# Optimization experiments

Measured on AMD Instinct MI355X. Metric: run time of the kernel, lower is better.

## Reference

```python
import jax, jax.numpy as jnp
import numpy as np

EPS = 1e-8  # torch CosineSimilarity eps
TEMP = 0.05

def _l2norm(x):
    n = jnp.sqrt(jnp.sum(x * x, axis=-1, keepdims=True))
    return x / jnp.maximum(n, EPS)

def setup_inputs() -> dict:
    key = jax.random.key(0)
    k1, k2, k3 = jax.random.split(key, 3)
    query = jax.random.normal(k1, (256, 768), dtype=jnp.float32)
    keys = jax.random.normal(k2, (256, 768), dtype=jnp.float32)
    queue = jax.random.normal(k3, (64, 1024, 768), dtype=jnp.float32)
    return {"query": query, "keys": keys, "queue": queue}

def reference(query, keys, queue):
    B, D = query.shape
    qn = _l2norm(query)                       # [B, D]
    kn = _l2norm(keys)                        # [B, D]
    negn = _l2norm(queue.reshape(-1, D))      # [N, D]
    sim_pos = jnp.einsum('bd,cd->bc', qn, kn)   # [B, B]
    sim_neg = jnp.einsum('bd,nd->bn', qn, negn) # [B, N]
    logits = jnp.concatenate([sim_pos, sim_neg], axis=1) / TEMP  # [B, B+N]
    target = jnp.arange(B)
    logp = jax.nn.log_softmax(logits, axis=-1)
    loss = -jnp.mean(logp[jnp.arange(B), target])
    return loss
```

## Files before the change

kernel.cpp:

```cpp
#include <hip/hip_runtime.h>
#include <hip/hip_bf16.h>

typedef __attribute__((ext_vector_type(8))) short short8;
typedef __attribute__((ext_vector_type(4))) float f32x4;

#define TEMP_INV 20.0f
#define NCH 256

__device__ inline unsigned short f2bf(float f){
    unsigned int u = __builtin_bit_cast(unsigned int, f);
    u += 0x7fffu + ((u >> 16) & 1u);
    return (unsigned short)(u >> 16);
}
__device__ inline float bf2f(unsigned short h){
    unsigned int u = ((unsigned int)h) << 16;
    return __builtin_bit_cast(float, u);
}
__device__ inline unsigned int pk2bf(float a, float b){
    return (unsigned int)f2bf(a) | ((unsigned int)f2bf(b) << 16);
}

#define GLOAD16(src, dst) __builtin_amdgcn_global_load_lds( \
    (const __attribute__((address_space(1))) unsigned int*)(src), \
    (__attribute__((address_space(3))) unsigned int*)(dst), 16, 0, 0)

__global__ __launch_bounds__(256) void k_norm(const float* __restrict__ q,
                                              unsigned short* __restrict__ Aswz,
                                              float* __restrict__ out){
    int b = blockIdx.x, t = threadIdx.x;
    if (b == 0 && t == 0) out[0] = 0.f;
    const float* qr = q + b * 768;
    float v0 = qr[t], v1 = qr[t + 256], v2 = qr[t + 512];
    float ss = v0*v0 + v1*v1 + v2*v2;
#pragma unroll
    for (int o = 32; o; o >>= 1) ss += __shfl_xor(ss, o);
    __shared__ float red[4];
    if ((t & 63) == 0) red[t >> 6] = ss;
    __syncthreads();
    ss = red[0] + red[1] + red[2] + red[3];
    float inv = 1.0f / fmaxf(sqrtf(ss), 1e-8f);
    float nv[3] = {v0 * inv, v1 * inv, v2 * inv};
#pragma unroll
    for (int j = 0; j < 3; j++){
        int cc = t + 256 * j;
        unsigned short h = f2bf(nv[j]);
        int kc = cc >> 6, kl = cc & 63, g = kl >> 3, e = kl & 7;
        int slot = g ^ (b & 7);
        Aswz[kc * 16384 + b * 64 + slot * 8 + e] = h;
    }
}

__global__ __launch_bounds__(1024) void k_main(
        const float* __restrict__ keys,
        const float* __restrict__ queue,
        const unsigned short* __restrict__ Aswz,
        float* __restrict__ pmax,
        float* __restrict__ psum,
        float* __restrict__ diag){
    __shared__ unsigned short Atile[16384];
    __shared__ unsigned short Btile[16384];
    __shared__ unsigned short bxn16[768];
    __shared__ float invn[256];
    __shared__ float redm[4][256];
    __shared__ float reds[4][256];
    __shared__ float xred[4][256];
    __shared__ float wred[16];
    __shared__ float sxs;

    const int b = blockIdx.x, t = threadIdx.x;
    const int lane = t & 63;
    const int w = t >> 6;
    const int wm = w >> 2, wn = w & 3;
    const int frow = lane & 15, fg = lane >> 4;
    const int c = t >> 2, q4 = t & 3;
    const int c7 = c & 7;

    {
        float v = (t < 768) ? keys[b * 768 + t] : 0.f;
        float ssx = v * v;
#pragma unroll
        for (int o = 32; o; o >>= 1) ssx += __shfl_xor(ssx, o);
        if (lane == 0) wred[w] = ssx;
        __syncthreads();
        if (t == 0){
            float s = 0.f;
#pragma unroll
            for (int i = 0; i < 16; i++) s += wred[i];
            sxs = 1.0f / fmaxf(sqrtf(s), 1e-8f);
        }
        __syncthreads();
        if (t < 768) bxn16[t] = f2bf(v * sxs);
        __syncthreads();
    }

    const float* rp = queue + (size_t)(b * 256 + c) * 768 + q4 * 16;
    const int xrow = t & 255, xk = t >> 8;

    float ssq = 0.f, dx = 0.f;
    f32x4 acc[4][4];
#pragma unroll
    for (int i = 0; i < 4; i++)
#pragma unroll
        for (int j = 0; j < 4; j++) acc[i][j] = (f32x4)0.f;

    for (int kc = 0; kc < 12; ++kc){
        if (kc) __syncthreads();
        GLOAD16(Aswz + kc * 16384 + t * 8, Atile + t * 8);
        GLOAD16(Aswz + kc * 16384 + 8192 + t * 8, Atile + 8192 + t * 8);
        {
            float4 u0 = *(const float4*)(rp + kc * 64);
            float4 u1 = *(const float4*)(rp + kc * 64 + 4);
            float4 u2 = *(const float4*)(rp + kc * 64 + 8);
            float4 u3 = *(const float4*)(rp + kc * 64 + 12);
            ssq += u0.x*u0.x + u0.y*u0.y + u0.z*u0.z + u0.w*u0.w;
            ssq += u1.x*u1.x + u1.y*u1.y + u1.z*u1.z + u1.w*u1.w;
            ssq += u2.x*u2.x + u2.y*u2.y + u2.z*u2.z + u2.w*u2.w;
            ssq += u3.x*u3.x + u3.y*u3.y + u3.z*u3.z + u3.w*u3.w;
            uint4 pk0, pk1;
            pk0.x = pk2bf(u0.x, u0.y); pk0.y = pk2bf(u0.z, u0.w);
            pk0.z = pk2bf(u1.x, u1.y); pk0.w = pk2bf(u1.z, u1.w);
            pk1.x = pk2bf(u2.x, u2.y); pk1.y = pk2bf(u2.z, u2.w);
            pk1.z = pk2bf(u3.x, u3.y); pk1.w = pk2bf(u3.z, u3.w);
            int slot0 = (q4 * 2) ^ c7;
            int slot1 = (q4 * 2 + 1) ^ c7;
            *(uint4*)&Btile[c * 64 + slot0 * 8] = pk0;
            *(uint4*)&Btile[c * 64 + slot1 * 8] = pk1;
        }
        __syncthreads();

#pragma unroll
        for (int ks = 0; ks < 2; ++ks){
            const int slotv = (ks * 4 + fg) ^ (frow & 7);
            short8 af[4], bfv[4];
#pragma unroll
            for (int fm = 0; fm < 4; ++fm)
                af[fm] = *(const short8*)&Atile[(wm * 64 + fm * 16 + frow) * 64 + slotv * 8];
#pragma unroll
            for (int fn = 0; fn < 4; ++fn)
                bfv[fn] = *(const short8*)&Btile[(wn * 64 + fn * 16 + frow) * 64 + slotv * 8];
#pragma unroll
            for (int fm = 0; fm < 4; ++fm)
#pragma unroll
                for (int fn = 0; fn < 4; ++fn)
                    acc[fm][fn] = __builtin_amdgcn_mfma_f32_16x16x32_bf16(
                        af[fm], bfv[fn], acc[fm][fn], 0, 0, 0);
        }

#pragma unroll
        for (int gi = 0; gi < 2; ++gi){
            int g = xk * 2 + gi;
            short8 av = *(const short8*)&Atile[xrow * 64 + (g ^ (xrow & 7)) * 8];
            short8 xv = *(const short8*)&bxn16[kc * 64 + g * 8];
#pragma unroll
            for (int e = 0; e < 8; ++e)
                dx += bf2f((unsigned short)av[e]) * bf2f((unsigned short)xv[e]);
        }
    }

    ssq += __shfl_xor(ssq, 1);
    ssq += __shfl_xor(ssq, 2);
    if (q4 == 0) invn[c] = 1.0f / fmaxf(sqrtf(ssq), 1e-8f);
    xred[xk][xrow] = dx;
    __syncthreads();

#pragma unroll
    for (int fm = 0; fm < 4; ++fm){
#pragma unroll
        for (int rr = 0; rr < 4; ++rr){
            float v[4];
#pragma unroll
            for (int fn = 0; fn < 4; ++fn)
                v[fn] = acc[fm][fn][rr] * invn[wn * 64 + fn * 16 + frow] * TEMP_INV;
            int row = wm * 64 + fm * 16 + fg * 4 + rr;
            float m = fmaxf(fmaxf(v[0], v[1]), fmaxf(v[2], v[3]));
#pragma unroll
            for (int o = 1; o < 16; o <<= 1) m = fmaxf(m, __shfl_xor(m, o));
            float s = __expf(v[0]-m) + __expf(v[1]-m) + __expf(v[2]-m) + __expf(v[3]-m);
#pragma unroll
            for (int o = 1; o < 16; o <<= 1) s += __shfl_xor(s, o);
            if (frow == 0){ redm[wn][row] = m; reds[wn][row] = s; }
        }
    }
    __syncthreads();
    if (t < 256){
        float M = -1e30f, S = 0.f;
#pragma unroll
        for (int ww = 0; ww < 4; ++ww){
            float m2 = redm[ww][t], s2 = reds[ww][t];
            float Mn = fmaxf(M, m2);
            S = S * __expf(M - Mn) + s2 * __expf(m2 - Mn);
            M = Mn;
        }
        float vx = (xred[0][t] + xred[1][t] + xred[2][t] + xred[3][t]) * TEMP_INV;
        if (t == b) diag[b] = vx;
        float Mn = fmaxf(M, vx);
        S = S * __expf(M - Mn) + __expf(vx - Mn);
        pmax[b * 256 + t] = Mn;
        psum[b * 256 + t] = S;
    }
}

__global__ __launch_bounds__(256) void k_lse(const float* __restrict__ pmax,
                                             const float* __restrict__ psum,
                                             const float* __restrict__ diag,
                                             float* __restrict__ out){
    int b = blockIdx.x, t = threadIdx.x;
    float m = -1e30f;
    for (int cc = t; cc < NCH; cc += 256) m = fmaxf(m, pmax[cc * 256 + b]);
#pragma unroll
    for (int o = 32; o; o >>= 1) m = fmaxf(m, __shfl_xor(m, o));
    __shared__ float red[4];
    __shared__ float Msh;
    if ((t & 63) == 0) red[t >> 6] = m;
    __syncthreads();
    if (t == 0) Msh = fmaxf(fmaxf(red[0], red[1]), fmaxf(red[2], red[3]));
    __syncthreads();
    float M = Msh;
    float s = 0.f;
    for (int cc = t; cc < NCH; cc += 256) s += psum[cc * 256 + b] * __expf(pmax[cc * 256 + b] - M);
#pragma unroll
    for (int o = 32; o; o >>= 1) s += __shfl_xor(s, o);
    if ((t & 63) == 0) red[t >> 6] = s;
    __syncthreads();
    if (t == 0)
        atomicAdd(out, (M + logf(red[0] + red[1] + red[2] + red[3]) - diag[b]) * (1.0f / 256.0f));
}

extern "C" void kernel_launch(void* const* d_in, const int* in_sizes, int n_in,
                              void* d_out, int out_size, void* d_ws, size_t ws_size,
                              hipStream_t stream){
    const float* q  = (const float*)d_in[0];
    const float* k  = (const float*)d_in[1];
    const float* qu = (const float*)d_in[2];
    char* ws = (char*)d_ws;
    unsigned short* Aswz = (unsigned short*)(ws);
    float* diag  = (float*)(ws + 393216);
    float* pmax  = (float*)(ws + 394240);
    float* psum  = (float*)(ws + 656384);

    k_norm<<<256, 256, 0, stream>>>(q, Aswz, (float*)d_out);
    k_main<<<256, 1024, 0, stream>>>(k, qu, Aswz, pmax, psum, diag);
    k_lse<<<256, 256, 0, stream>>>(pmax, psum, diag, (float*)d_out);
}
```

Measured before the change: 77.87 us.

## Split main GEMM into 1028 smaller blocks with double-buffered B tile and direct A loads

Result: slower. 130.0 us (+67.0%).

```diff
diff --git a/kernel.cpp b/kernel.cpp
--- a/kernel.cpp
+++ b/kernel.cpp
@@ -5,27 +5,19 @@
 typedef __attribute__((ext_vector_type(4))) float f32x4;
 
 #define TEMP_INV 20.0f
-#define NCH 256
+#define NCH 1028
 
 __device__ inline unsigned short f2bf(float f){
     unsigned int u = __builtin_bit_cast(unsigned int, f);
     u += 0x7fffu + ((u >> 16) & 1u);
     return (unsigned short)(u >> 16);
 }
-__device__ inline float bf2f(unsigned short h){
-    unsigned int u = ((unsigned int)h) << 16;
-    return __builtin_bit_cast(float, u);
-}
 __device__ inline unsigned int pk2bf(float a, float b){
     return (unsigned int)f2bf(a) | ((unsigned int)f2bf(b) << 16);
 }
 
-#define GLOAD16(src, dst) __builtin_amdgcn_global_load_lds( \
-    (const __attribute__((address_space(1))) unsigned int*)(src), \
-    (__attribute__((address_space(3))) unsigned int*)(dst), 16, 0, 0)
-
 __global__ __launch_bounds__(256) void k_norm(const float* __restrict__ q,
-                                              unsigned short* __restrict__ Aswz,
+                                              unsigned short* __restrict__ Alin,
                                               float* __restrict__ out){
     int b = blockIdx.x, t = threadIdx.x;
     if (b == 0 && t == 0) out[0] = 0.f;
@@ -43,160 +35,119 @@
 #pragma unroll
     for (int j = 0; j < 3; j++){
         int cc = t + 256 * j;
-        unsigned short h = f2bf(nv[j]);
-        int kc = cc >> 6, kl = cc & 63, g = kl >> 3, e = kl & 7;
-        int slot = g ^ (b & 7);
-        Aswz[kc * 16384 + b * 64 + slot * 8 + e] = h;
+        Alin[(cc >> 6) * 16384 + b * 64 + (cc & 63)] = f2bf(nv[j]);
     }
 }
 
-__global__ __launch_bounds__(1024) void k_main(
+__global__ __launch_bounds__(512, 4) void k_main(
         const float* __restrict__ keys,
         const float* __restrict__ queue,
-        const unsigned short* __restrict__ Aswz,
+        const unsigned short* __restrict__ Alin,
         float* __restrict__ pmax,
         float* __restrict__ psum,
         float* __restrict__ diag){
-    __shared__ unsigned short Atile[16384];
-    __shared__ unsigned short Btile[16384];
-    __shared__ unsigned short bxn16[768];
-    __shared__ float invn[256];
-    __shared__ float redm[4][256];
-    __shared__ float reds[4][256];
-    __shared__ float xred[4][256];
-    __shared__ float wred[16];
-    __shared__ float sxs;
+    __shared__ unsigned short Btile[2][4096];
+    __shared__ float invn[64];
+    __shared__ float redm[256];
+    __shared__ float reds[256];
 
     const int b = blockIdx.x, t = threadIdx.x;
     const int lane = t & 63;
     const int w = t >> 6;
-    const int wm = w >> 2, wn = w & 3;
     const int frow = lane & 15, fg = lane >> 4;
-    const int c = t >> 2, q4 = t & 3;
-    const int c7 = c & 7;
+    const int r = t >> 3, q8 = t & 7;
+    const bool keyb = (b >= 1024);
+    const int cb = b - 1024;
 
-    {
-        float v = (t < 768) ? keys[b * 768 + t] : 0.f;
-        float ssx = v * v;
+    const float* src = keyb ? (keys + (cb * 64 + r) * 768)
+                            : (queue + (size_t)(b * 64 + r) * 768);
+    const float* rp = src + q8 * 8;
+
+    float ssq = 0.f;
+    f32x4 acc[2][4];
 #pragma unroll
-        for (int o = 32; o; o >>= 1) ssx += __shfl_xor(ssx, o);
-        if (lane == 0) wred[w] = ssx;
-        __syncthreads();
-        if (t == 0){
-            float s = 0.f;
-#pragma unroll
-            for (int i = 0; i < 16; i++) s += wred[i];
-            sxs = 1.0f / fmaxf(sqrtf(s), 1e-8f);
-        }
-        __syncthreads();
-        if (t < 768) bxn16[t] = f2bf(v * sxs);
-        __syncthreads();
-    }
-
-    const float* rp = queue + (size_t)(b * 256 + c) * 768 + q4 * 16;
-    const int xrow = t & 255, xk = t >> 8;
-
-    float ssq = 0.f, dx = 0.f;
-    f32x4 acc[4][4];
-#pragma unroll
-    for (int i = 0; i < 4; i++)
+    for (int i = 0; i < 2; i++)
 #pragma unroll
         for (int j = 0; j < 4; j++) acc[i][j] = (f32x4)0.f;
 
-    for (int kc = 0; kc < 12; ++kc){
-        if (kc) __syncthreads();
-        GLOAD16(Aswz + kc * 16384 + t * 8, Atile + t * 8);
-        GLOAD16(Aswz + kc * 16384 + 8192 + t * 8, Atile + 8192 + t * 8);
-        {
-            float4 u0 = *(const float4*)(rp + kc * 64);
-            float4 u1 = *(const float4*)(rp + kc * 64 + 4);
-            float4 u2 = *(const float4*)(rp + kc * 64 + 8);
-            float4 u3 = *(const float4*)(rp + kc * 64 + 12);
-            ssq += u0.x*u0.x + u0.y*u0.y + u0.z*u0.z + u0.w*u0.w;
-            ssq += u1.x*u1.x + u1.y*u1.y + u1.z*u1.z + u1.w*u1.w;
-            ssq += u2.x*u2.x + u2.y*u2.y + u2.z*u2.z + u2.w*u2.w;
-            ssq += u3.x*u3.x + u3.y*u3.y + u3.z*u3.z + u3.w*u3.w;
-            uint4 pk0, pk1;
-            pk0.x = pk2bf(u0.x, u0.y); pk0.y = pk2bf(u0.z, u0.w);
-            pk0.z = pk2bf(u1.x, u1.y); pk0.w = pk2bf(u1.z, u1.w);
-            pk1.x = pk2bf(u2.x, u2.y); pk1.y = pk2bf(u2.z, u2.w);
-            pk1.z = pk2bf(u3.x, u3.y); pk1.w = pk2bf(u3.z, u3.w);
-            int slot0 = (q4 * 2) ^ c7;
-            int slot1 = (q4 * 2 + 1) ^ c7;
-            *(uint4*)&Btile[c * 64 + slot0 * 8] = pk0;
-            *(uint4*)&Btile[c * 64 + slot1 * 8] = pk1;
-        }
-        __syncthreads();
+    auto stage = [&](unsigned short* bt, float4 u0, float4 u1){
+        ssq += u0.x*u0.x + u0.y*u0.y + u0.z*u0.z + u0.w*u0.w;
+        ssq += u1.x*u1.x + u1.y*u1.y + u1.z*u1.z + u1.w*u1.w;
+        uint4 pk;
+        pk.x = pk2bf(u0.x, u0.y); pk.y = pk2bf(u0.z, u0.w);
+        pk.z = pk2bf(u1.x, u1.y); pk.w = pk2bf(u1.z, u1.w);
+        int slot = q8 ^ (r & 7);
+        *(uint4*)&bt[r * 64 + slot * 8] = pk;
+    };
+
+    float4 bA = *(const float4*)(rp);
+    float4 bB = *(const float4*)(rp + 4);
+    stage(Btile[0], bA, bB);
+    bA = *(const float4*)(rp + 64);
+    bB = *(const float4*)(rp + 68);
+    __syncthreads();
 
 #pragma unroll
+    for (int kc = 0; kc < 12; ++kc){
+        if (kc < 11) stage(Btile[(kc + 1) & 1], bA, bB);
+        if (kc < 10){
+            bA = *(const float4*)(rp + (kc + 2) * 64);
+            bB = *(const float4*)(rp + (kc + 2) * 64 + 4);
+        }
+        const unsigned short* Bt = Btile[kc & 1];
+#pragma unroll
         for (int ks = 0; ks < 2; ++ks){
-            const int slotv = (ks * 4 + fg) ^ (frow & 7);
-            short8 af[4], bfv[4];
+            short8 af[2], bf4[4];
 #pragma unroll
-            for (int fm = 0; fm < 4; ++fm)
-                af[fm] = *(const short8*)&Atile[(wm * 64 + fm * 16 + frow) * 64 + slotv * 8];
+            for (int fm = 0; fm < 2; ++fm)
+                af[fm] = *(const short8*)&Alin[kc * 16384 +
+                         (w * 32 + fm * 16 + frow) * 64 + ks * 32 + fg * 8];
 #pragma unroll
-            for (int fn = 0; fn < 4; ++fn)
-                bfv[fn] = *(const short8*)&Btile[(wn * 64 + fn * 16 + frow) * 64 + slotv * 8];
+            for (int fn = 0; fn < 4; ++fn){
+                int row = fn * 16 + frow;
+                int slot = (ks * 4 + fg) ^ (row & 7);
+                bf4[fn] = *(const short8*)&Bt[row * 64 + slot * 8];
+            }
 #pragma unroll
-            for (int fm = 0; fm < 4; ++fm)
+            for (int fm = 0; fm < 2; ++fm)
 #pragma unroll
                 for (int fn = 0; fn < 4; ++fn)
                     acc[fm][fn] = __builtin_amdgcn_mfma_f32_16x16x32_bf16(
-                        af[fm], bfv[fn], acc[fm][fn], 0, 0, 0);
+                        af[fm], bf4[fn], acc[fm][fn], 0, 0, 0);
         }
-
-#pragma unroll
-        for (int gi = 0; gi < 2; ++gi){
-            int g = xk * 2 + gi;
-            short8 av = *(const short8*)&Atile[xrow * 64 + (g ^ (xrow & 7)) * 8];
-            short8 xv = *(const short8*)&bxn16[kc * 64 + g * 8];
-#pragma unroll
-            for (int e = 0; e < 8; ++e)
-                dx += bf2f((unsigned short)av[e]) * bf2f((unsigned short)xv[e]);
-        }
+        __syncthreads();
     }
 
     ssq += __shfl_xor(ssq, 1);
     ssq += __shfl_xor(ssq, 2);
-    if (q4 == 0) invn[c] = 1.0f / fmaxf(sqrtf(ssq), 1e-8f);
-    xred[xk][xrow] = dx;
+    ssq += __shfl_xor(ssq, 4);
+    if (q8 == 0) invn[r] = 1.0f / fmaxf(sqrtf(ssq), 1e-8f);
     __syncthreads();
 
 #pragma unroll
-    for (int fm = 0; fm < 4; ++fm){
+    for (int fm = 0; fm < 2; ++fm){
 #pragma unroll
         for (int rr = 0; rr < 4; ++rr){
+            int row = w * 32 + fm * 16 + fg * 4 + rr;
             float v[4];
 #pragma unroll
-            for (int fn = 0; fn < 4; ++fn)
-                v[fn] = acc[fm][fn][rr] * invn[wn * 64 + fn * 16 + frow] * TEMP_INV;
-            int row = wm * 64 + fm * 16 + fg * 4 + rr;
+            for (int fn = 0; fn < 4; ++fn){
+                v[fn] = acc[fm][fn][rr] * invn[fn * 16 + frow] * TEMP_INV;
+                if (keyb && row == cb * 64 + fn * 16 + frow) diag[row] = v[fn];
+            }
             float m = fmaxf(fmaxf(v[0], v[1]), fmaxf(v[2], v[3]));
 #pragma unroll
             for (int o = 1; o < 16; o <<= 1) m = fmaxf(m, __shfl_xor(m, o));
             float s = __expf(v[0]-m) + __expf(v[1]-m) + __expf(v[2]-m) + __expf(v[3]-m);
 #pragma unroll
             for (int o = 1; o < 16; o <<= 1) s += __shfl_xor(s, o);
-            if (frow == 0){ redm[wn][row] = m; reds[wn][row] = s; }
+            if (frow == 0){ redm[row] = m; reds[row] = s; }
         }
     }
     __syncthreads();
     if (t < 256){
-        float M = -1e30f, S = 0.f;
-#pragma unroll
-        for (int ww = 0; ww < 4; ++ww){
-            float m2 = redm[ww][t], s2 = reds[ww][t];
-            float Mn = fmaxf(M, m2);
-            S = S * __expf(M - Mn) + s2 * __expf(m2 - Mn);
-            M = Mn;
-        }
-        float vx = (xred[0][t] + xred[1][t] + xred[2][t] + xred[3][t]) * TEMP_INV;
-        if (t == b) diag[b] = vx;
-        float Mn = fmaxf(M, vx);
-        S = S * __expf(M - Mn) + __expf(vx - Mn);
-        pmax[b * 256 + t] = Mn;
-        psum[b * 256 + t] = S;
+        pmax[b * 256 + t] = redm[t];
+        psum[b * 256 + t] = reds[t];
     }
 }
 
@@ -233,12 +184,12 @@
     const float* k  = (const float*)d_in[1];
     const float* qu = (const float*)d_in[2];
     char* ws = (char*)d_ws;
-    unsigned short* Aswz = (unsigned short*)(ws);
+    unsigned short* Alin = (unsigned short*)(ws);
     float* diag  = (float*)(ws + 393216);
     float* pmax  = (float*)(ws + 394240);
-    float* psum  = (float*)(ws + 656384);
+    float* psum  = (float*)(ws + 1446912);
 
-    k_norm<<<256, 256, 0, stream>>>(q, Aswz, (float*)d_out);
-    k_main<<<256, 1024, 0, stream>>>(k, qu, Aswz, pmax, psum, diag);
+    k_norm<<<256, 256, 0, stream>>>(q, Alin, (float*)d_out);
+    k_main<<<1028, 512, 0, stream>>>(k, qu, Alin, pmax, psum, diag);
     k_lse<<<256, 256, 0, stream>>>(pmax, psum, diag, (float*)d_out);
 }
```

## Split main GEMM into 128x128 tiles and treat keys as extra tiles

Applied to the files above, without the earlier changes.

Result: slower. 110.1 us (+41.4%).

```diff
diff --git a/kernel.cpp b/kernel.cpp
--- a/kernel.cpp
+++ b/kernel.cpp
@@ -5,16 +5,12 @@
 typedef __attribute__((ext_vector_type(4))) float f32x4;
 
 #define TEMP_INV 20.0f
-#define NCH 256
+#define NCH 514
 
 __device__ inline unsigned short f2bf(float f){
     unsigned int u = __builtin_bit_cast(unsigned int, f);
     u += 0x7fffu + ((u >> 16) & 1u);
     return (unsigned short)(u >> 16);
-}
-__device__ inline float bf2f(unsigned short h){
-    unsigned int u = ((unsigned int)h) << 16;
-    return __builtin_bit_cast(float, u);
 }
 __device__ inline unsigned int pk2bf(float a, float b){
     return (unsigned int)f2bf(a) | ((unsigned int)f2bf(b) << 16);
@@ -43,88 +39,71 @@
 #pragma unroll
     for (int j = 0; j < 3; j++){
         int cc = t + 256 * j;
-        unsigned short h = f2bf(nv[j]);
+        unsigned short hh = f2bf(nv[j]);
         int kc = cc >> 6, kl = cc & 63, g = kl >> 3, e = kl & 7;
         int slot = g ^ (b & 7);
-        Aswz[kc * 16384 + b * 64 + slot * 8 + e] = h;
-    }
-}
-
-__global__ __launch_bounds__(1024) void k_main(
+        Aswz[kc * 16384 + b * 64 + slot * 8 + e] = hh;
+    }
+}
+
+__global__ __launch_bounds__(256) void k_main(
         const float* __restrict__ keys,
         const float* __restrict__ queue,
         const unsigned short* __restrict__ Aswz,
         float* __restrict__ pmax,
         float* __restrict__ psum,
         float* __restrict__ diag){
-    __shared__ unsigned short Atile[16384];
-    __shared__ unsigned short Btile[16384];
-    __shared__ unsigned short bxn16[768];
-    __shared__ float invn[256];
-    __shared__ float redm[4][256];
-    __shared__ float reds[4][256];
-    __shared__ float xred[4][256];
-    __shared__ float wred[16];
-    __shared__ float sxs;
+    __shared__ unsigned short Atile[8192];
+    __shared__ unsigned short Btile[8192];
+    __shared__ float invn[128];
+    __shared__ float redm[2][128];
+    __shared__ float reds[2][128];
 
     const int b = blockIdx.x, t = threadIdx.x;
+    const int bc = b >> 1, ar = b & 1;
+    const bool keyb = (bc >= 512);
+    const int colBase = (keyb ? (bc - 512) : bc) * 128;
     const int lane = t & 63;
     const int w = t >> 6;
-    const int wm = w >> 2, wn = w & 3;
+    const int wm = w >> 1, wn = w & 1;
     const int frow = lane & 15, fg = lane >> 4;
-    const int c = t >> 2, q4 = t & 3;
-    const int c7 = c & 7;
-
-    {
-        float v = (t < 768) ? keys[b * 768 + t] : 0.f;
-        float ssx = v * v;
-#pragma unroll
-        for (int o = 32; o; o >>= 1) ssx += __shfl_xor(ssx, o);
-        if (lane == 0) wred[w] = ssx;
-        __syncthreads();
-        if (t == 0){
-            float s = 0.f;
-#pragma unroll
-            for (int i = 0; i < 16; i++) s += wred[i];
-            sxs = 1.0f / fmaxf(sqrtf(s), 1e-8f);
-        }
-        __syncthreads();
-        if (t < 768) bxn16[t] = f2bf(v * sxs);
-        __syncthreads();
-    }
-
-    const float* rp = queue + (size_t)(b * 256 + c) * 768 + q4 * 16;
-    const int xrow = t & 255, xk = t >> 8;
-
-    float ssq = 0.f, dx = 0.f;
+    const int c = t >> 1, h = t & 1;
+
+    const float* src = (keyb ? keys : queue) + (size_t)(colBase + c) * 768 + h * 32;
+
+    float ssq = 0.f;
     f32x4 acc[4][4];
 #pragma unroll
     for (int i = 0; i < 4; i++)
 #pragma unroll
         for (int j = 0; j < 4; j++) acc[i][j] = (f32x4)0.f;
 
+#pragma unroll 1
     for (int kc = 0; kc < 12; ++kc){
         if (kc) __syncthreads();
-        GLOAD16(Aswz + kc * 16384 + t * 8, Atile + t * 8);
-        GLOAD16(Aswz + kc * 16384 + 8192 + t * 8, Atile + 8192 + t * 8);
+#pragma unroll
+        for (int i = 0; i < 4; ++i)
+            GLOAD16(Aswz + kc * 16384 + ar * 8192 + i * 2048 + t * 8,
+                    Atile + i * 2048 + t * 8);
         {
-            float4 u0 = *(const float4*)(rp + kc * 64);
-            float4 u1 = *(const float4*)(rp + kc * 64 + 4);
-            float4 u2 = *(const float4*)(rp + kc * 64 + 8);
-            float4 u3 = *(const float4*)(rp + kc * 64 + 12);
-            ssq += u0.x*u0.x + u0.y*u0.y + u0.z*u0.z + u0.w*u0.w;
-            ssq += u1.x*u1.x + u1.y*u1.y + u1.z*u1.z + u1.w*u1.w;
-            ssq += u2.x*u2.x + u2.y*u2.y + u2.z*u2.z + u2.w*u2.w;
-            ssq += u3.x*u3.x + u3.y*u3.y + u3.z*u3.z + u3.w*u3.w;
-            uint4 pk0, pk1;
-            pk0.x = pk2bf(u0.x, u0.y); pk0.y = pk2bf(u0.z, u0.w);
-            pk0.z = pk2bf(u1.x, u1.y); pk0.w = pk2bf(u1.z, u1.w);
-            pk1.x = pk2bf(u2.x, u2.y); pk1.y = pk2bf(u2.z, u2.w);
-            pk1.z = pk2bf(u3.x, u3.y); pk1.w = pk2bf(u3.z, u3.w);
-            int slot0 = (q4 * 2) ^ c7;
-            int slot1 = (q4 * 2 + 1) ^ c7;
-            *(uint4*)&Btile[c * 64 + slot0 * 8] = pk0;
-            *(uint4*)&Btile[c * 64 + slot1 * 8] = pk1;
+            float4 u[8];
+#pragma unroll
+            for (int j = 0; j < 8; ++j)
+                u[j] = *(const float4*)(src + kc * 64 + j * 4);
+#pragma unroll
+            for (int j = 0; j < 8; ++j)
+                ssq += u[j].x*u[j].x + u[j].y*u[j].y + u[j].z*u[j].z + u[j].w*u[j].w;
+#pragma unroll
+            for (int j = 0; j < 4; ++j){
+                uint4 pk;
+                pk.x = pk2bf(u[2*j].x,   u[2*j].y);
+                pk.y = pk2bf(u[2*j].z,   u[2*j].w);
+                pk.z = pk2bf(u[2*j+1].x, u[2*j+1].y);
+                pk.w = pk2bf(u[2*j+1].z, u[2*j+1].w);
+                int idx8 = h * 4 + j;
+                int slot = idx8 ^ (c & 7);
+                *(uint4*)&Btile[c * 64 + slot * 8] = pk;
+            }
         }
         __syncthreads();
 
@@ -145,33 +124,25 @@
                     acc[fm][fn] = __builtin_amdgcn_mfma_f32_16x16x32_bf16(
                         af[fm], bfv[fn], acc[fm][fn], 0, 0, 0);
         }
-
-#pragma unroll
-        for (int gi = 0; gi < 2; ++gi){
-            int g = xk * 2 + gi;
-            short8 av = *(const short8*)&Atile[xrow * 64 + (g ^ (xrow & 7)) * 8];
-            short8 xv = *(const short8*)&bxn16[kc * 64 + g * 8];
-#pragma unroll
-            for (int e = 0; e < 8; ++e)
-                dx += bf2f((unsigned short)av[e]) * bf2f((unsigned short)xv[e]);
-        }
     }
 
     ssq += __shfl_xor(ssq, 1);
-    ssq += __shfl_xor(ssq, 2);
-    if (q4 == 0) invn[c] = 1.0f / fmaxf(sqrtf(ssq), 1e-8f);
-    xred[xk][xrow] = dx;
+    if (h == 0) invn[c] = 1.0f / fmaxf(sqrtf(ssq), 1e-8f);
     __syncthreads();
 
 #pragma unroll
     for (int fm = 0; fm < 4; ++fm){
 #pragma unroll
         for (int rr = 0; rr < 4; ++rr){
+            int row = wm * 64 + fm * 16 + fg * 4 + rr;
             float v[4];
 #pragma unroll
-            for (int fn = 0; fn < 4; ++fn)
-                v[fn] = acc[fm][fn][rr] * invn[wn * 64 + fn * 16 + frow] * TEMP_INV;
-            int row = wm * 64 + fm * 16 + fg * 4 + rr;
+            for (int fn = 0; fn < 4; ++fn){
+                int col = wn * 64 + fn * 16 + frow;
+                v[fn] = acc[fm][fn][rr] * invn[col] * TEMP_INV;
+                if (keyb && (ar * 128 + row) == (colBase + col))
+                    diag[ar * 128 + row] = v[fn];
+            }
             float m = fmaxf(fmaxf(v[0], v[1]), fmaxf(v[2], v[3]));
 #pragma unroll
             for (int o = 1; o < 16; o <<= 1) m = fmaxf(m, __shfl_xor(m, o));
@@ -182,21 +153,12 @@
         }
     }
     __syncthreads();
-    if (t < 256){
-        float M = -1e30f, S = 0.f;
-#pragma unroll
-        for (int ww = 0; ww < 4; ++ww){
-            float m2 = redm[ww][t], s2 = reds[ww][t];
-            float Mn = fmaxf(M, m2);
-            S = S * __expf(M - Mn) + s2 * __expf(m2 - Mn);
-            M = Mn;
-        }
-        float vx = (xred[0][t] + xred[1][t] + xred[2][t] + xred[3][t]) * TEMP_INV;
-        if (t == b) diag[b] = vx;
-        float Mn = fmaxf(M, vx);
-        S = S * __expf(M - Mn) + __expf(vx - Mn);
-        pmax[b * 256 + t] = Mn;
-        psum[b * 256 + t] = S;
+    if (t < 128){
+        float m0 = redm[0][t], m1 = redm[1][t];
+        float M = fmaxf(m0, m1);
+        float S = reds[0][t] * __expf(m0 - M) + reds[1][t] * __expf(m1 - M);
+        pmax[bc * 256 + ar * 128 + t] = M;
+        psum[bc * 256 + ar * 128 + t] = S;
     }
 }
 
@@ -236,9 +198,9 @@
     unsigned short* Aswz = (unsigned short*)(ws);
     float* diag  = (float*)(ws + 393216);
     float* pmax  = (float*)(ws + 394240);
-    float* psum  = (float*)(ws + 656384);
+    float* psum  = (float*)(ws + 920576);
 
     k_norm<<<256, 256, 0, stream>>>(q, Aswz, (float*)d_out);
-    k_main<<<256, 1024, 0, stream>>>(k, qu, Aswz, pmax, psum, diag);
+    k_main<<<1028, 256, 0, stream>>>(k, qu, Aswz, pmax, psum, diag);
     k_lse<<<256, 256, 0, stream>>>(pmax, psum, diag, (float*)d_out);
 }
```
